# Performance work log

Hardware: AMD Instinct MI355X
Metric: run time of the kernel (lower is better)

Reference implementation:

```python
import jax, jax.numpy as jnp
import numpy as np

B, S, D, H = 4, 1024, 512, 8
DH = D // H  # 64 head dim; max_len == S for the masked (preceding_only) skew path


def setup_inputs() -> dict:
    key = jax.random.key(0)
    ks = jax.random.split(key, 8)
    queries = jax.random.normal(ks[0], (B, S, D), jnp.float32)
    keys_ = jax.random.normal(ks[1], (B, S, D), jnp.float32)
    values = jax.random.normal(ks[2], (B, S, D), jnp.float32)
    Wq = jax.random.normal(ks[3], (D, D), jnp.float32) * 0.03
    Wk = jax.random.normal(ks[4], (D, D), jnp.float32) * 0.03
    Wv = jax.random.normal(ks[5], (D, D), jnp.float32) * 0.03
    Wo = jax.random.normal(ks[6], (D, D), jnp.float32) * 0.03
    rel_emb = jax.random.normal(ks[7], (H, DH, S), jnp.float32) * 0.03  # preceding_only -> len == max_len
    i = jnp.arange(S)
    mask = jnp.where(i[None, :] > i[:, None], -1e9, 0.0).astype(jnp.float32)[None, None]  # [1,1,S,S] causal
    return {"queries": queries, "keys": keys_, "values": values, "mask": mask,
            "Wq": Wq, "Wk": Wk, "Wv": Wv, "Wo": Wo, "rel_emb": rel_emb}


def _skewed_rel_bias(q, rel_emb):
    # q: [B,H,S,DH], rel_emb: [H,DH,L] with L == max_len == S
    b, h, s, _ = q.shape
    L = rel_emb.shape[-1]
    qe = jnp.einsum('bhsd,hdl->bhsl', q, rel_emb)  # [B,H,S,L]
    # _qe_masking: keep qe[..., i, j] where j >= L-1-i
    lengths = (L - 1) - jnp.arange(s)
    keep = (jnp.arange(L)[None, :] >= lengths[:, None]).astype(qe.dtype)
    qe = qe * keep
    # skew: pad one column on the left, fold into [B,H,L+1,S], drop first row
    qe = jnp.pad(qe, ((0, 0), (0, 0), (0, 0), (1, 0)))
    qe = qe.reshape(b, h, L + 1, s)[:, :, 1:, :]  # [B,H,L,S]
    return qe


def reference(queries, keys, values, mask, Wq, Wk, Wv, Wo, rel_emb):
    b, s, _ = queries.shape
    h, dh, _ = rel_emb.shape
    scale = dh ** -0.5

    def split(x):  # [B,S,H*DH] -> [B,H,S,DH]
        return x.reshape(b, s, h, dh).transpose(0, 2, 1, 3)

    q = split(queries @ Wq)
    k = split(keys @ Wk)
    v = split(values @ Wv)

    logits = jnp.einsum('bhsd,bhtd->bhst', q, k)
    logits = logits + _skewed_rel_bias(q, rel_emb)
    logits = (logits + mask[:, :, :s, :s]) * scale  # original scales after adding mask
    weights = jax.nn.softmax(logits, axis=-1)
    ctx = jnp.einsum('bhst,bhtd->bhsd', weights, v)
    ctx = ctx.transpose(0, 2, 1, 3).reshape(b, s, h * dh)
    return ctx @ Wo
```

## Files before the change

kernel.cpp:

```cpp
#include <hip/hip_runtime.h>
#include <hip/hip_bf16.h>

#define SB 4
#define SS 1024
#define SD 512
#define SH 8
#define SDH 64

typedef short bf16x8 __attribute__((ext_vector_type(8)));
typedef float f32x4 __attribute__((ext_vector_type(4)));

#define MFMA(a, b, c) __builtin_amdgcn_mfma_f32_16x16x32_bf16(a, b, c, 0, 0, 0)

__device__ __forceinline__ void load_lds16(const void* g, void* l) {
  __builtin_amdgcn_global_load_lds(
      (__attribute__((address_space(1))) void*)(const_cast<void*>(g)),
      (__attribute__((address_space(3))) void*)(l), 16, 0, 0);
}

__global__ __launch_bounds__(256) void k_prep(
    const float* __restrict__ q, const float* __restrict__ k, const float* __restrict__ v,
    const float* __restrict__ Wq, const float* __restrict__ Wk, const float* __restrict__ Wv,
    const float* __restrict__ Wo, const float* __restrict__ rel,
    __hip_bfloat16* __restrict__ Xq, __hip_bfloat16* __restrict__ Xk,
    __hip_bfloat16* __restrict__ Xv, __hip_bfloat16* __restrict__ Wqt,
    __hip_bfloat16* __restrict__ Wkt, __hip_bfloat16* __restrict__ Wvt,
    __hip_bfloat16* __restrict__ Wot, __hip_bfloat16* __restrict__ relT) {
  __shared__ float tile[32][33];
  const int y = blockIdx.y, x = blockIdx.x, t = threadIdx.x;
  if (y < 3) {
    const float2* in = (const float2*)(y == 0 ? q : y == 1 ? k : v);
    __hip_bfloat162* out = (__hip_bfloat162*)(y == 0 ? Xq : y == 1 ? Xk : Xv);
    const int n2 = SB * SS * SD / 2;
    int i = x * 256 + t, st = 512 * 256;
    for (; i < n2; i += st) out[i] = __float22bfloat162_rn(in[i]);
    return;
  }
  int tx = t & 31, ty = t >> 5;
  if (y < 5) {
    int which = (y - 3) * 2 + (x >> 8), idx = x & 255;
    const float* ip = which == 0 ? Wq : which == 1 ? Wk : which == 2 ? Wv : Wo;
    __hip_bfloat16* op = which == 0 ? Wqt : which == 1 ? Wkt : which == 2 ? Wvt : Wot;
    int c0 = (idx & 15) * 32, r0 = (idx >> 4) * 32;
    for (int rr = ty; rr < 32; rr += 8) tile[rr][tx] = ip[(size_t)(r0 + rr) * SD + c0 + tx];
    __syncthreads();
    for (int cc = ty; cc < 32; cc += 8)
      op[(size_t)(c0 + cc) * SD + r0 + tx] = __float2bfloat16(tile[tx][cc]);
    return;
  }
  int hd = x >> 6, idx = x & 63;
  int c0 = (idx >> 1) * 32, r0 = (idx & 1) * 32;
  const float* ip = rel + (size_t)hd * SDH * SS;
  __hip_bfloat16* op = relT + (size_t)hd * SDH * SS;
  for (int rr = ty; rr < 32; rr += 8) tile[rr][tx] = ip[(size_t)(r0 + rr) * SS + c0 + tx];
  __syncthreads();
  for (int cc = ty; cc < 32; cc += 8)
    op[(size_t)(c0 + cc) * SDH + r0 + tx] = __float2bfloat16(tile[tx][cc]);
}

__global__ __launch_bounds__(256) void k_gemm_qkv(
    const __hip_bfloat16* __restrict__ Xq, const __hip_bfloat16* __restrict__ Xk,
    const __hip_bfloat16* __restrict__ Xv, const __hip_bfloat16* __restrict__ Wqt,
    const __hip_bfloat16* __restrict__ Wkt, const __hip_bfloat16* __restrict__ Wvt,
    __hip_bfloat16* __restrict__ Qb, __hip_bfloat16* __restrict__ Kb,
    __hip_bfloat16* __restrict__ Vt) {
  __shared__ __hip_bfloat16 As[128 * 64];
  __shared__ __hip_bfloat16 Bs[128 * 64];
  const int z = blockIdx.z;
  const __hip_bfloat16* A = z == 0 ? Xq : z == 1 ? Xk : Xv;
  const __hip_bfloat16* Bt = z == 0 ? Wqt : z == 1 ? Wkt : Wvt;
  __hip_bfloat16* Cout = z == 0 ? Qb : z == 1 ? Kb : Vt;
  const int mode = (z == 2) ? 1 : 0;
  const int t = threadIdx.x, w = t >> 6, lane = t & 63;
  const int quad = lane >> 4, l16 = lane & 15;
  const int m0 = blockIdx.y * 128, n0 = blockIdx.x * 128;
  const int wm = (w >> 1) * 64, wn = (w & 1) * 64;
  f32x4 zero4 = {0.0f, 0.0f, 0.0f, 0.0f};
  f32x4 acc[4][4];
#pragma unroll
  for (int mi = 0; mi < 4; ++mi)
#pragma unroll
    for (int nj = 0; nj < 4; ++nj) acc[mi][nj] = zero4;

  for (int kt = 0; kt < SD; kt += 64) {
#pragma unroll
    for (int c = 0; c < 4; ++c) {
      int ofs = c * 256 + t;
      int row = ofs >> 3, col = (ofs & 7) ^ (row & 7);
      load_lds16(A + (size_t)(m0 + row) * SD + kt + col * 8,
                 (char*)As + (size_t)(c * 256 + w * 64) * 16);
      load_lds16(Bt + (size_t)(n0 + row) * SD + kt + col * 8,
                 (char*)Bs + (size_t)(c * 256 + w * 64) * 16);
    }
    __syncthreads();
    bf16x8 af[4][2], bfr[4][2];
#pragma unroll
    for (int mi = 0; mi < 4; ++mi) {
      int row = wm + mi * 16 + l16;
#pragma unroll
      for (int ks = 0; ks < 2; ++ks)
        af[mi][ks] = *(const bf16x8*)((const char*)As + row * 128 +
                                      ((ks * 4 + quad) ^ (row & 7)) * 16);
    }
#pragma unroll
    for (int nj = 0; nj < 4; ++nj) {
      int row = wn + nj * 16 + l16;
#pragma unroll
      for (int ks = 0; ks < 2; ++ks)
        bfr[nj][ks] = *(const bf16x8*)((const char*)Bs + row * 128 +
                                       ((ks * 4 + quad) ^ (row & 7)) * 16);
    }
#pragma unroll
    for (int mi = 0; mi < 4; ++mi)
#pragma unroll
      for (int nj = 0; nj < 4; ++nj) {
        acc[mi][nj] = MFMA(af[mi][0], bfr[nj][0], acc[mi][nj]);
        acc[mi][nj] = MFMA(af[mi][1], bfr[nj][1], acc[mi][nj]);
      }
    __syncthreads();
  }
#pragma unroll
  for (int mi = 0; mi < 4; ++mi)
#pragma unroll
    for (int nj = 0; nj < 4; ++nj)
#pragma unroll
      for (int r = 0; r < 4; ++r) {
        int m = m0 + wm + mi * 16 + quad * 4 + r;
        int n = n0 + wn + nj * 16 + l16;
        int b = m >> 10, s = m & 1023, hh = n >> 6, dh = n & 63;
        __hip_bfloat16 bv = __float2bfloat16(acc[mi][nj][r]);
        if (mode == 0)
          Cout[((size_t)(b * SH + hh) * SS + s) * SDH + dh] = bv;
        else
          Cout[((size_t)(b * SH + hh) * SDH + dh) * SS + s] = bv;
      }
}

__global__ __launch_bounds__(256) void k_gemm_o(const __hip_bfloat16* __restrict__ A,
                                                const __hip_bfloat16* __restrict__ Bt,
                                                float* __restrict__ Out) {
  __shared__ __hip_bfloat16 As[128 * 64];
  __shared__ __hip_bfloat16 Bs[64 * 64];
  const int t = threadIdx.x, w = t >> 6, lane = t & 63;
  const int quad = lane >> 4, l16 = lane & 15;
  const int m0 = blockIdx.y * 128, n0 = blockIdx.x * 64;
  const int wm = (w >> 1) * 64, wn = (w & 1) * 32;
  f32x4 zero4 = {0.0f, 0.0f, 0.0f, 0.0f};
  f32x4 acc[4][2];
#pragma unroll
  for (int mi = 0; mi < 4; ++mi)
#pragma unroll
    for (int nj = 0; nj < 2; ++nj) acc[mi][nj] = zero4;

  for (int kt = 0; kt < SD; kt += 64) {
#pragma unroll
    for (int c = 0; c < 4; ++c) {
      int ofs = c * 256 + t;
      int row = ofs >> 3, col = (ofs & 7) ^ (row & 7);
      load_lds16(A + (size_t)(m0 + row) * SD + kt + col * 8,
                 (char*)As + (size_t)(c * 256 + w * 64) * 16);
    }
#pragma unroll
    for (int c = 0; c < 2; ++c) {
      int ofs = c * 256 + t;
      int row = ofs >> 3, col = (ofs & 7) ^ (row & 7);
      load_lds16(Bt + (size_t)(n0 + row) * SD + kt + col * 8,
                 (char*)Bs + (size_t)(c * 256 + w * 64) * 16);
    }
    __syncthreads();
    bf16x8 af[4][2], bfr[2][2];
#pragma unroll
    for (int mi = 0; mi < 4; ++mi) {
      int row = wm + mi * 16 + l16;
#pragma unroll
      for (int ks = 0; ks < 2; ++ks)
        af[mi][ks] = *(const bf16x8*)((const char*)As + row * 128 +
                                      ((ks * 4 + quad) ^ (row & 7)) * 16);
    }
#pragma unroll
    for (int nj = 0; nj < 2; ++nj) {
      int row = wn + nj * 16 + l16;
#pragma unroll
      for (int ks = 0; ks < 2; ++ks)
        bfr[nj][ks] = *(const bf16x8*)((const char*)Bs + row * 128 +
                                       ((ks * 4 + quad) ^ (row & 7)) * 16);
    }
#pragma unroll
    for (int mi = 0; mi < 4; ++mi)
#pragma unroll
      for (int nj = 0; nj < 2; ++nj) {
        acc[mi][nj] = MFMA(af[mi][0], bfr[nj][0], acc[mi][nj]);
        acc[mi][nj] = MFMA(af[mi][1], bfr[nj][1], acc[mi][nj]);
      }
    __syncthreads();
  }
#pragma unroll
  for (int mi = 0; mi < 4; ++mi)
#pragma unroll
    for (int nj = 0; nj < 2; ++nj)
#pragma unroll
      for (int r = 0; r < 4; ++r) {
        int m = m0 + wm + mi * 16 + quad * 4 + r;
        int n = n0 + wn + nj * 16 + l16;
        Out[(size_t)m * SD + n] = acc[mi][nj][r];
      }
}

__global__ __launch_bounds__(256) void k_flash(const __hip_bfloat16* __restrict__ Qb,
                                               const __hip_bfloat16* __restrict__ Kb,
                                               const __hip_bfloat16* __restrict__ Vt,
                                               const __hip_bfloat16* __restrict__ relT,
                                               float* __restrict__ Opart,
                                               float* __restrict__ lpart,
                                               __hip_bfloat16* __restrict__ CTX) {
  __shared__ __hip_bfloat16 Klds[64 * 64];
  __shared__ __hip_bfloat16 Vlds[64 * 64];
  __shared__ __hip_bfloat16 REs[128 * 64];
  __shared__ __hip_bfloat16 QEP[64 * 136];
  const int t = threadIdx.x, w = t >> 6, lane = t & 63;
  const int quad = lane >> 4, l16 = lane & 15;
  const int idx = blockIdx.x, bh = blockIdx.y, h = bh & 7;
  int tI, c, jt0, nt;
  bool single;
  if (idx < 16) {
    tI = 8 + (idx >> 1); c = idx & 1;
    jt0 = c ? 8 : 0; nt = c ? (tI - 7) : 8; single = false;
  } else {
    tI = idx - 16; c = 0; jt0 = 0; nt = tI + 1; single = true;
  }
  const int i0 = tI * 64;
  const size_t qbase = (size_t)bh * SS * SDH;
  const __hip_bfloat16* Rp = relT + (size_t)h * SS * SDH;

  const int qrow = i0 + w * 16 + l16;
  bf16x8 qf0 = *(const bf16x8*)(Qb + qbase + (size_t)qrow * SDH + quad * 8);
  bf16x8 qf1 = *(const bf16x8*)(Qb + qbase + (size_t)qrow * SDH + 32 + quad * 8);

  f32x4 zero4 = {0.0f, 0.0f, 0.0f, 0.0f};
  f32x4 acc_o[4];
#pragma unroll
  for (int dt = 0; dt < 4; ++dt) acc_o[dt] = zero4;
  float ls[4] = {0.0f, 0.0f, 0.0f, 0.0f};
  const int rloc = quad * 4;
  __hip_bfloat16* myrow = QEP + (size_t)(w * 16 + rloc) * 136;

  for (int jt = 0; jt < nt; ++jt) {
    const int jtile = jt0 + jt, j0 = jtile * 64;
    const int l0 = 960 - 64 * (tI - jtile);
    const int m64 = l0 >> 6;
    const int ph_lo = m64 & 1, ph_hi = 1 - ph_lo;
    const bool first = (jt == 0);
#pragma unroll
    for (int cc = 0; cc < 2; ++cc) {
      int ofs = cc * 256 + t;
      int row = ofs >> 3, col = (ofs & 7) ^ (row & 7);
      load_lds16(Kb + qbase + (size_t)(j0 + row) * SDH + col * 8,
                 (char*)Klds + (size_t)(cc * 256 + w * 64) * 16);
      load_lds16(Vt + (size_t)bh * SDH * SS + (size_t)row * SS + j0 + col * 8,
                 (char*)Vlds + (size_t)(cc * 256 + w * 64) * 16);
    }
#pragma unroll
    for (int cc = 0; cc < 2; ++cc) {
      int ofs = cc * 256 + t;
      int row = ofs >> 3, col = (ofs & 7) ^ (row & 7);
      int lr = l0 + 64 + row;
      if (lr > 1023) lr = 1023;
      load_lds16(Rp + (size_t)lr * SDH + col * 8,
                 (char*)REs + ph_hi * 8192 + (size_t)(cc * 256 + w * 64) * 16);
    }
    if (first) {
#pragma unroll
      for (int cc = 0; cc < 2; ++cc) {
        int ofs = cc * 256 + t;
        int row = ofs >> 3, col = (ofs & 7) ^ (row & 7);
        int lr = l0 + row;
        load_lds16(Rp + (size_t)lr * SDH + col * 8,
                   (char*)REs + ph_lo * 8192 + (size_t)(cc * 256 + w * 64) * 16);
      }
    }
    __syncthreads();

    f32x4 s[4];
#pragma unroll
    for (int nj = 0; nj < 4; ++nj) {
      int row = nj * 16 + l16;
      bf16x8 b0 = *(const bf16x8*)((const char*)Klds + row * 128 + (quad ^ (row & 7)) * 16);
      bf16x8 b1 = *(const bf16x8*)((const char*)Klds + row * 128 + ((4 + quad) ^ (row & 7)) * 16);
      f32x4 z = zero4;
      z = MFMA(qf0, b0, z);
      z = MFMA(qf1, b1, z);
      s[nj] = z;
    }
#pragma unroll
    for (int nc = 0; nc < 8; ++nc) {
      if (nc < 4 && !first) continue;
      int ph = (m64 + (nc >> 2)) & 1;
      int prow = ph * 64 + (nc & 3) * 16 + l16;
      bf16x8 b0 = *(const bf16x8*)((const char*)REs + prow * 128 + ((quad ^ (prow & 7))) * 16);
      bf16x8 b1 = *(const bf16x8*)((const char*)REs + prow * 128 + (((4 + quad) ^ (prow & 7))) * 16);
      f32x4 e = zero4;
      e = MFMA(qf0, b0, e);
      e = MFMA(qf1, b1, e);
#pragma unroll
      for (int r = 0; r < 4; ++r)
        myrow[r * 136 + ph * 64 + (nc & 3) * 16 + l16] = __float2bfloat16(e[r]);
    }

#pragma unroll
    for (int nj = 0; nj < 4; ++nj) {
      int jc = nj * 16 + l16, jcol = j0 + jc;
#pragma unroll
      for (int r = 0; r < 4; ++r) {
        int irow = i0 + w * 16 + rloc + r;
        int off = 63 + jc - (rloc + r);
        int pcol = ((m64 + (off >> 6)) & 1) * 64 + (off & 63);
        float bias = __bfloat162float(myrow[r * 136 + pcol]);
        float val = (s[nj][r] + bias) * 0.125f - 8.0f;
        float p = (jcol <= irow) ? __expf(val) : 0.0f;
        s[nj][r] = p;
        ls[r] += p;
      }
    }
    const int pc = ph_lo * 64;
#pragma unroll
    for (int nj = 0; nj < 4; ++nj)
#pragma unroll
      for (int r = 0; r < 4; ++r)
        myrow[r * 136 + pc + nj * 16 + l16] = __float2bfloat16(s[nj][r]);

#pragma unroll
    for (int js = 0; js < 2; ++js) {
      bf16x8 pa = *(const bf16x8*)(QEP + (size_t)(w * 16 + l16) * 136 + pc +
                                   js * 32 + quad * 8);
#pragma unroll
      for (int dt = 0; dt < 4; ++dt) {
        int row = dt * 16 + l16;
        bf16x8 vb = *(const bf16x8*)((const char*)Vlds + row * 128 +
                                     ((js * 4 + quad) ^ (row & 7)) * 16);
        acc_o[dt] = MFMA(pa, vb, acc_o[dt]);
      }
    }
    __syncthreads();
  }
  float rsum[4];
#pragma unroll
  for (int r = 0; r < 4; ++r) {
    float sum = ls[r];
    sum += __shfl_xor(sum, 1, 64);
    sum += __shfl_xor(sum, 2, 64);
    sum += __shfl_xor(sum, 4, 64);
    sum += __shfl_xor(sum, 8, 64);
    rsum[r] = sum;
  }
  if (single) {
    const int b = bh >> 3;
#pragma unroll
    for (int r = 0; r < 4; ++r) {
      int row = w * 16 + rloc + r;
      float rl = 1.0f / rsum[r];
#pragma unroll
      for (int dt = 0; dt < 4; ++dt)
        CTX[((size_t)b * SS + i0 + row) * SD + h * SDH + dt * 16 + l16] =
            __float2bfloat16(acc_o[dt][r] * rl);
    }
  } else {
    const size_t pbase = ((size_t)bh * 8 + (tI - 8)) * 2 + c;
    float* Op = Opart + pbase * 4096;
#pragma unroll
    for (int r = 0; r < 4; ++r) {
      int row = w * 16 + rloc + r;
#pragma unroll
      for (int dt = 0; dt < 4; ++dt) Op[row * 64 + dt * 16 + l16] = acc_o[dt][r];
      if (l16 == 0) lpart[pbase * 64 + row] = rsum[r];
    }
  }
}

__global__ __launch_bounds__(256) void k_reduce2(const float* __restrict__ Opart,
                                                 const float* __restrict__ lpart,
                                                 __hip_bfloat16* __restrict__ CTX) {
  const int bx = blockIdx.x, bh = blockIdx.y, b = bh >> 3, h = bh & 7;
  const int tI = 8 + bx, tid = threadIdx.x;
  __shared__ float lsum[64];
  const size_t base = ((size_t)bh * 8 + bx) * 2;
  if (tid < 64) lsum[tid] = lpart[base * 64 + tid] + lpart[(base + 1) * 64 + tid];
  __syncthreads();
  const int e0 = tid * 16, row = e0 >> 6, d0 = e0 & 63;
  const float4* p0 = (const float4*)(Opart + base * 4096);
  const float4* p1 = (const float4*)(Opart + (base + 1) * 4096);
  const float rl = 1.0f / lsum[row];
  __hip_bfloat16* op = CTX + ((size_t)b * SS + tI * 64 + row) * SD + h * SDH + d0;
#pragma unroll
  for (int vv = 0; vv < 4; ++vv) {
    float4 x = p0[tid * 4 + vv], y = p1[tid * 4 + vv];
    op[vv * 4 + 0] = __float2bfloat16((x.x + y.x) * rl);
    op[vv * 4 + 1] = __float2bfloat16((x.y + y.y) * rl);
    op[vv * 4 + 2] = __float2bfloat16((x.z + y.z) * rl);
    op[vv * 4 + 3] = __float2bfloat16((x.w + y.w) * rl);
  }
}

extern "C" void kernel_launch(void* const* d_in, const int* in_sizes, int n_in,
                              void* d_out, int out_size, void* d_ws, size_t ws_size,
                              hipStream_t stream) {
  const float* queries = (const float*)d_in[0];
  const float* keys    = (const float*)d_in[1];
  const float* values  = (const float*)d_in[2];
  const float* Wq = (const float*)d_in[4];
  const float* Wk = (const float*)d_in[5];
  const float* Wv = (const float*)d_in[6];
  const float* Wo = (const float*)d_in[7];
  const float* rel = (const float*)d_in[8];

  char* ws = (char*)d_ws;
  size_t off = 0;
  auto alloc = [&](size_t bytes) {
    char* p = ws + off;
    off += (bytes + 255) & ~(size_t)255;
    return p;
  };
  const size_t XB = (size_t)SB * SS * SD * 2;
  const size_t WB = (size_t)SD * SD * 2;
  __hip_bfloat16* Wqt  = (__hip_bfloat16*)alloc(WB);
  __hip_bfloat16* Wkt  = (__hip_bfloat16*)alloc(WB);
  __hip_bfloat16* Wvt  = (__hip_bfloat16*)alloc(WB);
  __hip_bfloat16* Wot  = (__hip_bfloat16*)alloc(WB);
  __hip_bfloat16* relT = (__hip_bfloat16*)alloc((size_t)SH * SS * SDH * 2);
  __hip_bfloat16* Qb   = (__hip_bfloat16*)alloc(XB);
  __hip_bfloat16* Kb   = (__hip_bfloat16*)alloc(XB);
  __hip_bfloat16* Vt   = (__hip_bfloat16*)alloc(XB);
  __hip_bfloat16* CTX  = (__hip_bfloat16*)alloc(XB);
  char* uni = alloc(3 * XB);
  __hip_bfloat16* Xq = (__hip_bfloat16*)uni;
  __hip_bfloat16* Xk = (__hip_bfloat16*)(uni + XB);
  __hip_bfloat16* Xv = (__hip_bfloat16*)(uni + 2 * XB);
  float* Opart = (float*)uni;
  float* lpart = (float*)(uni + (size_t)32 * 8 * 2 * 4096 * 4);
  if (off > ws_size) return;

  k_prep<<<dim3(512, 6), dim3(256), 0, stream>>>(
      queries, keys, values, Wq, Wk, Wv, Wo, rel,
      Xq, Xk, Xv, Wqt, Wkt, Wvt, Wot, relT);
  k_gemm_qkv<<<dim3(SD / 128, SB * SS / 128, 3), dim3(256), 0, stream>>>(
      Xq, Xk, Xv, Wqt, Wkt, Wvt, Qb, Kb, Vt);
  k_flash<<<dim3(24, SB * SH), dim3(256), 0, stream>>>(Qb, Kb, Vt, relT, Opart, lpart, CTX);
  k_reduce2<<<dim3(8, SB * SH), dim3(256), 0, stream>>>(Opart, lpart, CTX);
  k_gemm_o<<<dim3(SD / 64, SB * SS / 128), dim3(256), 0, stream>>>(CTX, Wot, (float*)d_out);
}
```

Baseline: 150.9 us.

## Prefetch next K/V/rel tiles into registers to overlap loads with compute

Replaces the direct global-to-LDS loads in the attention loop with register prefetching. The next tile's K, V and relative-embedding data are loaded into registers while the current tile's MFMA work runs, then written to LDS at the top of the next iteration. The aim is to hide global memory latency behind compute. In exchange it uses more registers, which may lower occupancy, and it moves the barrier to the top of the loop.

```diff
diff --git a/kernel.cpp b/kernel.cpp
--- a/kernel.cpp
+++ b/kernel.cpp
@@ -230,11 +230,34 @@
   }
   const int i0 = tI * 64;
   const size_t qbase = (size_t)bh * SS * SDH;
+  const size_t vbase = (size_t)bh * SDH * SS;
   const __hip_bfloat16* Rp = relT + (size_t)h * SS * SDH;
 
   const int qrow = i0 + w * 16 + l16;
   bf16x8 qf0 = *(const bf16x8*)(Qb + qbase + (size_t)qrow * SDH + quad * 8);
   bf16x8 qf1 = *(const bf16x8*)(Qb + qbase + (size_t)qrow * SDH + 32 + quad * 8);
+
+  int srow[2], scol[2];
+#pragma unroll
+  for (int cc = 0; cc < 2; ++cc) {
+    int ofs = cc * 256 + t;
+    srow[cc] = ofs >> 3;
+    scol[cc] = (ofs & 7) ^ (srow[cc] & 7);
+  }
+
+  bf16x8 pk[2], pv[2], pr[2], prlo[2];
+  {
+    const int j0 = jt0 * 64, l0 = 960 - 64 * (tI - jt0);
+#pragma unroll
+    for (int cc = 0; cc < 2; ++cc) {
+      pk[cc] = *(const bf16x8*)(Kb + qbase + (size_t)(j0 + srow[cc]) * SDH + scol[cc] * 8);
+      pv[cc] = *(const bf16x8*)(Vt + vbase + (size_t)srow[cc] * SS + j0 + scol[cc] * 8);
+      int lr = l0 + 64 + srow[cc];
+      if (lr > 1023) lr = 1023;
+      pr[cc] = *(const bf16x8*)(Rp + (size_t)lr * SDH + scol[cc] * 8);
+      prlo[cc] = *(const bf16x8*)(Rp + (size_t)(l0 + srow[cc]) * SDH + scol[cc] * 8);
+    }
+  }
 
   f32x4 zero4 = {0.0f, 0.0f, 0.0f, 0.0f};
   f32x4 acc_o[4];
@@ -250,35 +273,32 @@
     const int m64 = l0 >> 6;
     const int ph_lo = m64 & 1, ph_hi = 1 - ph_lo;
     const bool first = (jt == 0);
+
+    if (!first) __syncthreads();
 #pragma unroll
     for (int cc = 0; cc < 2; ++cc) {
-      int ofs = cc * 256 + t;
-      int row = ofs >> 3, col = (ofs & 7) ^ (row & 7);
-      load_lds16(Kb + qbase + (size_t)(j0 + row) * SDH + col * 8,
-                 (char*)Klds + (size_t)(cc * 256 + w * 64) * 16);
-      load_lds16(Vt + (size_t)bh * SDH * SS + (size_t)row * SS + j0 + col * 8,
-                 (char*)Vlds + (size_t)(cc * 256 + w * 64) * 16);
-    }
-#pragma unroll
-    for (int cc = 0; cc < 2; ++cc) {
-      int ofs = cc * 256 + t;
-      int row = ofs >> 3, col = (ofs & 7) ^ (row & 7);
-      int lr = l0 + 64 + row;
-      if (lr > 1023) lr = 1023;
-      load_lds16(Rp + (size_t)lr * SDH + col * 8,
-                 (char*)REs + ph_hi * 8192 + (size_t)(cc * 256 + w * 64) * 16);
+      ((bf16x8*)Klds)[cc * 256 + t] = pk[cc];
+      ((bf16x8*)Vlds)[cc * 256 + t] = pv[cc];
+      ((bf16x8*)REs)[ph_hi * 512 + cc * 256 + t] = pr[cc];
     }
     if (first) {
 #pragma unroll
+      for (int cc = 0; cc < 2; ++cc)
+        ((bf16x8*)REs)[ph_lo * 512 + cc * 256 + t] = prlo[cc];
+    }
+    __syncthreads();
+
+    if (jt + 1 < nt) {
+      const int j0n = j0 + 64, l0n = l0 + 64;
+#pragma unroll
       for (int cc = 0; cc < 2; ++cc) {
-        int ofs = cc * 256 + t;
-        int row = ofs >> 3, col = (ofs & 7) ^ (row & 7);
-        int lr = l0 + row;
-        load_lds16(Rp + (size_t)lr * SDH + col * 8,
-                   (char*)REs + ph_lo * 8192 + (size_t)(cc * 256 + w * 64) * 16);
-      }
-    }
-    __syncthreads();
+        pk[cc] = *(const bf16x8*)(Kb + qbase + (size_t)(j0n + srow[cc]) * SDH + scol[cc] * 8);
+        pv[cc] = *(const bf16x8*)(Vt + vbase + (size_t)srow[cc] * SS + j0n + scol[cc] * 8);
+        int lr = l0n + 64 + srow[cc];
+        if (lr > 1023) lr = 1023;
+        pr[cc] = *(const bf16x8*)(Rp + (size_t)lr * SDH + scol[cc] * 8);
+      }
+    }
 
     f32x4 s[4];
 #pragma unroll
@@ -340,7 +360,6 @@
         acc_o[dt] = MFMA(pa, vb, acc_o[dt]);
       }
     }
-    __syncthreads();
   }
   float rsum[4];
 #pragma unroll
```

New measurement: 155.4 us. 3.0% more time.
